# Kernel optimization log

Hardware: AMD Instinct MI355X
Metric: run time of the kernel (lower is better)

The kernel has to match this reference:

```python
import jax, jax.numpy as jnp
import numpy as np

B, N = 32, 64
IMG_H, IMG_W = 1024, 1024
LEVEL_SIZES = [(128, 128), (64, 64), (32, 32), (16, 16), (8, 8)]
EPS = 1e-7


def setup_inputs() -> dict:
    key = jax.random.key(0)
    ks = jax.random.split(key, 12)
    inp = {}
    for i, (h, w) in enumerate(LEVEL_SIZES):
        inp[f"att{i}"] = jax.random.uniform(ks[i], (B, 1, h, w), jnp.float32, 0.01, 0.99)
    # boxes: centers uniform in image, sides log-uniform in [24, 700] px
    cx = jax.random.uniform(ks[5], (B, N)) * IMG_W
    cy = jax.random.uniform(ks[6], (B, N)) * IMG_H
    bw = jnp.exp(jax.random.uniform(ks[7], (B, N), minval=jnp.log(24.0), maxval=jnp.log(700.0)))
    bh = jnp.exp(jax.random.uniform(ks[8], (B, N), minval=jnp.log(24.0), maxval=jnp.log(700.0)))
    x1 = jnp.clip(cx - bw / 2, 0.0, IMG_W - 2.0)
    y1 = jnp.clip(cy - bh / 2, 0.0, IMG_H - 2.0)
    x2 = jnp.clip(cx + bw / 2, x1 + 1.0, float(IMG_W))
    y2 = jnp.clip(cy + bh / 2, y1 + 1.0, float(IMG_H))
    lab = jnp.where(jax.random.uniform(ks[9], (B, N)) < 0.1, -1.0, 0.0)
    inp["bboxs"] = jnp.stack([x1, y1, x2, y2, lab], axis=-1).astype(jnp.float32)
    inp["H"] = IMG_H
    inp["W"] = IMG_W
    return inp


def _loss(atts, bboxs, H, W):
    x1, y1, x2, y2, lab = (bboxs[..., k] for k in range(5))  # each [B,N]
    valid = (lab != -1) & (x1 <= W) & (y1 <= H) & (x2 <= W) & (y2 <= H)
    area = (x2 - x1) * (y2 - y1)
    has_valid = jnp.any(valid, axis=1)  # [B]
    level_losses = []
    for lid, att in enumerate(atts):
        h, w = att.shape[2], att.shape[3]
        base = float(2 ** (lid + 5))
        min_a = base ** 2 * 0.5
        max_a = (base * 1.58) ** 2 * 2.0
        lv = valid & (area >= min_a) & (area <= max_a)  # [B,N]
        # scale box coords into attention-map pixel space
        sx = w / W
        sy = h / H
        ix1 = jnp.maximum(jnp.floor(x1 * sx), 0.0)
        iy1 = jnp.maximum(jnp.floor(y1 * sy), 0.0)
        ix2 = jnp.minimum(jnp.ceil(x2 * sx) + 1.0, float(w))
        iy2 = jnp.minimum(jnp.ceil(y2 * sy) + 1.0, float(h))
        ys = jnp.arange(h, dtype=jnp.float32)
        xs = jnp.arange(w, dtype=jnp.float32)
        y_in = (lv[:, :, None] & (ys >= iy1[:, :, None]) & (ys < iy2[:, :, None])).astype(jnp.float32)  # [B,N,h]
        x_in = ((xs >= ix1[:, :, None]) & (xs < ix2[:, :, None])).astype(jnp.float32)  # [B,N,w]
        # rasterized GT: pixel covered by any selected box
        mask_gt = (jnp.einsum('bnh,bnw->bhw', y_in, x_in) > 0).astype(att.dtype)  # [B,h,w]
        p = jnp.clip(att[:, 0], EPS, 1.0 - EPS)  # [B,h,w]
        bce = -(mask_gt * jnp.log(p) + (1.0 - mask_gt) * jnp.log1p(-p))
        level_losses.append(bce.mean(axis=(1, 2)))  # [B]
    per_img = jnp.stack(level_losses, axis=0).mean(axis=0)  # mean over levels, [B]
    per_img = jnp.where(has_valid, per_img, 0.0)  # images with no valid boxes -> 0
    return per_img.mean(keepdims=True)  # shape [1]


def reference(att0, att1, att2, att3, att4, bboxs, H, W):
    return _loss([att0, att1, att2, att3, att4], bboxs, H, W)
```

## Files before the change

kernel.cpp:

```cpp
#include <hip/hip_runtime.h>

#define NBOX 64
#define BLK  256

__device__ __forceinline__ unsigned long long range_mask(int x1, int x2, int base) {
    int lo = max(x1 - base, 0);
    int hi = min(x2 - base, 64);
    if (lo >= hi) return 0ull;
    unsigned long long m = (~0ull) >> (64 - (hi - lo));
    return m << lo;
}

__global__ __launch_bounds__(BLK) void level_loss_partial(
    const float* __restrict__ att0, const float* __restrict__ att1,
    const float* __restrict__ att2, const float* __restrict__ att3,
    const float* __restrict__ att4,
    const float* __restrict__ bboxs,
    const int* __restrict__ Hp, const int* __restrict__ Wp,
    float* __restrict__ partial, int B)
{
    __shared__ unsigned long long smask[64][2];
    __shared__ int    s_hasvalid;
    __shared__ double sred[BLK];

    const int tid  = threadIdx.x;
    const int bid  = blockIdx.x;
    const int b    = bid >> 3;
    const int slot = bid & 7;
    const int lid   = (slot < 4) ? 0 : (slot - 3);
    const int chunk = (slot < 4) ? slot : 0;
    const int lw  = 7 - lid;
    const int w   = 1 << lw;
    const int npx = w << lw;
    const int start = chunk * 4096;
    const int end   = min(npx, start + 4096);
    const int r0    = start >> lw;
    const int nrows = (end - start) >> lw;

    const float Hf = (float)(*Hp);
    const float Wf = (float)(*Wp);

    if (tid < 64) {
        smask[tid][0] = 0ull;
        smask[tid][1] = 0ull;

        const float* bb = bboxs + ((size_t)b * NBOX + tid) * 5;
        const float x1 = bb[0], y1 = bb[1], x2 = bb[2], y2 = bb[3], lab = bb[4];
        const bool valid = (lab != -1.0f) && (x1 <= Wf) && (y1 <= Hf)
                        && (x2 <= Wf) && (y2 <= Hf);
        const float area = (x2 - x1) * (y2 - y1);
        const float base = (float)(32 << lid);
        const float min_a = base * base * 0.5f;
        const double bd   = (double)base * 1.58;
        const float max_a = (float)(bd * bd * 2.0);
        const bool lv = valid && (area >= min_a) && (area <= max_a);

        const unsigned long long mvalid = __ballot(valid);
        if (tid == 0) s_hasvalid = (mvalid != 0ull) ? 1 : 0;

        if (lv) {
            const float sx = (float)w / Wf;
            const float sy = (float)w / Hf;
            const int ix1 = (int)fmaxf(floorf(x1 * sx), 0.0f);
            const int iy1 = (int)fmaxf(floorf(y1 * sy), 0.0f);
            const int ix2 = (int)fminf(ceilf(x2 * sx) + 1.0f, (float)w);
            const int iy2 = (int)fminf(ceilf(y2 * sy) + 1.0f, (float)w);
            const int ys = max(iy1, r0);
            const int ye = min(iy2, r0 + nrows);
            const unsigned long long m0 = range_mask(ix1, ix2, 0);
            const unsigned long long m1 = range_mask(ix1, ix2, 64);
            for (int y = ys; y < ye; ++y) {
                if (m0) atomicOr(&smask[y - r0][0], m0);
                if (m1) atomicOr(&smask[y - r0][1], m1);
            }
        }
    }
    __syncthreads();

    const float* att = (lid == 0) ? att0 : (lid == 1) ? att1
                     : (lid == 2) ? att2 : (lid == 3) ? att3 : att4;
    const float* attb = att + (size_t)b * npx;

    const float lo_c = 1e-7f;
    const float hi_c = (float)(1.0 - 1e-7);

    double acc = 0.0;
    for (int p0 = start + tid * 4; p0 < end; p0 += BLK * 4) {
        const float4 a = *reinterpret_cast<const float4*>(attb + p0);
        const int y  = p0 >> lw;
        const int x0 = p0 & (w - 1);
        const unsigned int bits =
            (unsigned int)(smask[y - r0][(x0 >> 6) & 1] >> (x0 & 63)) & 0xFu;
        const float v0 = fminf(fmaxf(a.x, lo_c), hi_c);
        const float v1 = fminf(fmaxf(a.y, lo_c), hi_c);
        const float v2 = fminf(fmaxf(a.z, lo_c), hi_c);
        const float v3 = fminf(fmaxf(a.w, lo_c), hi_c);
        acc += (bits & 1u) ? (double)(-logf(v0)) : (double)(-log1pf(-v0));
        acc += (bits & 2u) ? (double)(-logf(v1)) : (double)(-log1pf(-v1));
        acc += (bits & 4u) ? (double)(-logf(v2)) : (double)(-log1pf(-v2));
        acc += (bits & 8u) ? (double)(-logf(v3)) : (double)(-log1pf(-v3));
    }

    sred[tid] = acc;
    __syncthreads();
    for (int s = BLK / 2; s > 0; s >>= 1) {
        if (tid < s) sred[tid] += sred[tid + s];
        __syncthreads();
    }
    if (tid == 0) {
        const double wgt = s_hasvalid
            ? 1.0 / (5.0 * (double)B * (double)npx)
            : 0.0;
        partial[bid] = (float)(sred[0] * wgt);
    }
}

__global__ __launch_bounds__(256) void reduce_partials(
    const float* __restrict__ partial, int n, float* __restrict__ out)
{
    __shared__ double sred[256];
    const int tid = threadIdx.x;
    double a = 0.0;
    for (int i = tid; i < n; i += 256) a += (double)partial[i];
    sred[tid] = a;
    __syncthreads();
    for (int s = 128; s > 0; s >>= 1) {
        if (tid < s) sred[tid] += sred[tid + s];
        __syncthreads();
    }
    if (tid == 0) out[0] = (float)sred[0];
}

extern "C" void kernel_launch(void* const* d_in, const int* in_sizes, int n_in,
                              void* d_out, int out_size, void* d_ws, size_t ws_size,
                              hipStream_t stream) {
    const float* att0  = (const float*)d_in[0];
    const float* att1  = (const float*)d_in[1];
    const float* att2  = (const float*)d_in[2];
    const float* att3  = (const float*)d_in[3];
    const float* att4  = (const float*)d_in[4];
    const float* bboxs = (const float*)d_in[5];
    const int*   Hp    = (const int*)d_in[6];
    const int*   Wp    = (const int*)d_in[7];
    float* out = (float*)d_out;

    const int B = in_sizes[5] / (NBOX * 5);
    const int nblk = B * 8;
    float* partial = (float*)d_ws;

    level_loss_partial<<<nblk, BLK, 0, stream>>>(att0, att1, att2, att3, att4,
                                                 bboxs, Hp, Wp, partial, B);
    reduce_partials<<<1, 256, 0, stream>>>(partial, nblk, out);
}
```

Measured before the change: 76.59 us.

## Fuse partial and final reduction into one cooperative kernel with grid sync

Merges the per-block loss kernel and the single-block reduction kernel into one cooperative launch. Blocks publish double-precision partials with release stores, then the whole grid synchronises and block 0 sums them with acquire loads. The shared-memory tree reduction is also replaced by wave shuffles plus a four-entry shared combine. This removes a second kernel launch and several block barriers, at the cost of cooperative-launch overhead and a grid-wide barrier. The final reduce assumes there are at most 256 blocks.

```diff
diff --git a/kernel.cpp b/kernel.cpp
--- a/kernel.cpp
+++ b/kernel.cpp
@@ -1,4 +1,7 @@
 #include <hip/hip_runtime.h>
+#include <hip/hip_cooperative_groups.h>
+
+namespace cg = cooperative_groups;
 
 #define NBOX 64
 #define BLK  256
@@ -11,20 +14,27 @@
     return m << lo;
 }
 
-__global__ __launch_bounds__(BLK) void level_loss_partial(
+__device__ __forceinline__ double wave_reduce(double v) {
+    #pragma unroll
+    for (int m = 1; m < 64; m <<= 1) v += __shfl_xor(v, m, 64);
+    return v;
+}
+
+__global__ __launch_bounds__(BLK) void level_loss_fused(
     const float* __restrict__ att0, const float* __restrict__ att1,
     const float* __restrict__ att2, const float* __restrict__ att3,
     const float* __restrict__ att4,
     const float* __restrict__ bboxs,
     const int* __restrict__ Hp, const int* __restrict__ Wp,
-    float* __restrict__ partial, int B)
+    double* __restrict__ partial, float* __restrict__ out, int B)
 {
     __shared__ unsigned long long smask[64][2];
     __shared__ int    s_hasvalid;
-    __shared__ double sred[BLK];
+    __shared__ double swave[BLK / 64];
 
     const int tid  = threadIdx.x;
     const int bid  = blockIdx.x;
+    const int nblk = gridDim.x;
     const int b    = bid >> 3;
     const int slot = bid & 7;
     const int lid   = (slot < 4) ? 0 : (slot - 3);
@@ -101,34 +111,31 @@
         acc += (bits & 8u) ? (double)(-logf(v3)) : (double)(-log1pf(-v3));
     }
 
-    sred[tid] = acc;
+    acc = wave_reduce(acc);
+    if ((tid & 63) == 0) swave[tid >> 6] = acc;
     __syncthreads();
-    for (int s = BLK / 2; s > 0; s >>= 1) {
-        if (tid < s) sred[tid] += sred[tid + s];
-        __syncthreads();
-    }
     if (tid == 0) {
+        double s = swave[0] + swave[1] + swave[2] + swave[3];
         const double wgt = s_hasvalid
             ? 1.0 / (5.0 * (double)B * (double)npx)
             : 0.0;
-        partial[bid] = (float)(sred[0] * wgt);
+        __hip_atomic_store(&partial[bid], s * wgt,
+                           __ATOMIC_RELEASE, __HIP_MEMORY_SCOPE_AGENT);
     }
-}
 
-__global__ __launch_bounds__(256) void reduce_partials(
-    const float* __restrict__ partial, int n, float* __restrict__ out)
-{
-    __shared__ double sred[256];
-    const int tid = threadIdx.x;
-    double a = 0.0;
-    for (int i = tid; i < n; i += 256) a += (double)partial[i];
-    sred[tid] = a;
-    __syncthreads();
-    for (int s = 128; s > 0; s >>= 1) {
-        if (tid < s) sred[tid] += sred[tid + s];
+    cg::this_grid().sync();
+
+    if (bid == 0) {
+        double v = 0.0;
+        if (tid < nblk)
+            v = __hip_atomic_load(&partial[tid],
+                                  __ATOMIC_ACQUIRE, __HIP_MEMORY_SCOPE_AGENT);
+        v = wave_reduce(v);
+        if ((tid & 63) == 0) swave[tid >> 6] = v;
         __syncthreads();
+        if (tid == 0)
+            out[0] = (float)(swave[0] + swave[1] + swave[2] + swave[3]);
     }
-    if (tid == 0) out[0] = (float)sred[0];
 }
 
 extern "C" void kernel_launch(void* const* d_in, const int* in_sizes, int n_in,
@@ -142,13 +149,14 @@
     const float* bboxs = (const float*)d_in[5];
     const int*   Hp    = (const int*)d_in[6];
     const int*   Wp    = (const int*)d_in[7];
-    float* out = (float*)d_out;
+    float*  out     = (float*)d_out;
+    double* partial = (double*)d_ws;
+    int B = in_sizes[5] / (NBOX * 5);
+    int nblk = B * 8;
 
-    const int B = in_sizes[5] / (NBOX * 5);
-    const int nblk = B * 8;
-    float* partial = (float*)d_ws;
-
-    level_loss_partial<<<nblk, BLK, 0, stream>>>(att0, att1, att2, att3, att4,
-                                                 bboxs, Hp, Wp, partial, B);
-    reduce_partials<<<1, 256, 0, stream>>>(partial, nblk, out);
+    void* args[] = { (void*)&att0, (void*)&att1, (void*)&att2, (void*)&att3,
+                     (void*)&att4, (void*)&bboxs, (void*)&Hp, (void*)&Wp,
+                     (void*)&partial, (void*)&out, (void*)&B };
+    hipLaunchCooperativeKernel((void*)level_loss_fused,
+                               dim3(nblk), dim3(BLK), args, 0, stream);
 }
```

After: 129.4 us. 1.69x slower.
